# Performance work log

Measured on AMD Instinct MI355X. Metric: run time of the kernel, lower is better.

## Reference

```python
import jax, jax.numpy as jnp
import numpy as np

HIDDEN = 768
E_ROUTED = 32
K_ACT = 4
E_SHARED = 8
RANK = 64
FFN_ROUTED = HIDDEN * 2
FFN_SHARED = HIDDEN * 3


def setup_inputs() -> dict:
    key = jax.random.key(0)
    ks = jax.random.split(key, 8)
    s = 0.02
    return {
        "x": jax.random.normal(ks[0], (2, 2048, HIDDEN), dtype=jnp.float32),
        # shared experts: SwiGLU (gate, up, down), stacked over experts
        "shared_wg": jax.random.normal(ks[1], (E_SHARED, HIDDEN, FFN_SHARED), dtype=jnp.float32) * s,
        "shared_wu": jax.random.normal(ks[2], (E_SHARED, HIDDEN, FFN_SHARED), dtype=jnp.float32) * s,
        "shared_wd": jax.random.normal(ks[3], (E_SHARED, FFN_SHARED, HIDDEN), dtype=jnp.float32) * s,
        # routed experts: Linear -> GELU -> Linear, stacked
        "routed_w1": jax.random.normal(ks[4], (E_ROUTED, HIDDEN, FFN_ROUTED), dtype=jnp.float32) * s,
        "routed_w2": jax.random.normal(ks[5], (E_ROUTED, FFN_ROUTED, HIDDEN), dtype=jnp.float32) * s,
        # low-rank router
        "router_down": jax.random.normal(ks[6], (HIDDEN, RANK), dtype=jnp.float32) * s,
        "router_up": jax.random.normal(ks[7], (RANK, E_ROUTED), dtype=jnp.float32) * s,
    }


def reference(x, shared_wg, shared_wu, shared_wd, routed_w1, routed_w2, router_down, router_up):
    B, S, D = x.shape
    xf = x.reshape(-1, D)  # [T, D]

    # shared experts (SwiGLU), averaged
    g = jnp.einsum('td,edh->eth', xf, shared_wg)
    u = jnp.einsum('td,edh->eth', xf, shared_wu)
    sh = jnp.einsum('eth,ehd->etd', jax.nn.silu(g) * u, shared_wd)
    shared_output = sh.mean(axis=0)  # [T, D] (sum / num_shared_expert)

    # low-rank router + top-k
    router_logits = (xf @ router_down) @ router_up  # [T, E]
    routing_weights, selected = jax.lax.top_k(router_logits, K_ACT)  # [T, K]
    routing_weights = jax.nn.softmax(routing_weights, axis=-1)

    # dense all-expert FFN (faithful to source), then gather top-k (== one-hot einsum)
    h = jnp.einsum('td,edh->eth', xf, routed_w1)
    expert_outputs = jnp.einsum('eth,ehd->etd', jax.nn.gelu(h, approximate=False), routed_w2)  # [E,T,D]
    sel_out = jnp.take_along_axis(expert_outputs.transpose(1, 0, 2), selected[:, :, None], axis=1)  # [T,K,D]
    routed_output = jnp.einsum('tkd,tk->td', sel_out, routing_weights)

    output = (shared_output + routed_output).reshape(B, S, D)

    # aux losses
    counts = jnp.bincount(selected.reshape(-1), length=E_ROUTED).astype(jnp.float32)
    load_balance_loss = jnp.var(counts, ddof=1)  # torch .var() is unbiased
    probs = jax.nn.softmax(router_logits, axis=-1)
    router_entropy = -(probs * jnp.log(probs + 1e-10)).sum(-1).mean()
    shared_norm = jnp.linalg.norm(shared_output, axis=-1).mean()
    routed_norm = jnp.linalg.norm(routed_output, axis=-1).mean()
    balance_loss = jnp.abs(shared_norm - routed_norm)

    return output, load_balance_loss, router_entropy, balance_loss
```

## Files before the change

kernel.cpp:

```cpp
#include <hip/hip_runtime.h>
#include <hip/hip_bf16.h>
#include <math.h>


#define T_TOK 4096
#define DHID 768
#define NE_R 32
#define NE_S 8
#define F_S 2304
#define F_R 1536
#define MAXROWS 20480
#define MAX_TILES 160

typedef float f32x4 __attribute__((ext_vector_type(4)));
typedef short s16x8 __attribute__((ext_vector_type(8)));

__device__ __forceinline__ short f2bf(float f) {
  union { float f; unsigned u; } v; v.f = f;
  unsigned r = v.u + 0x7fffu + ((v.u >> 16) & 1u);
  return (short)(r >> 16);
}

#define GLD16(gsrc, ldst)                                                     \
  __builtin_amdgcn_global_load_lds(                                           \
      (const __attribute__((address_space(1))) void*)(gsrc),                  \
      (__attribute__((address_space(3))) void*)(ldst), 16, 0, 0)

__global__ __launch_bounds__(256) void cvt_x_kernel(const float* __restrict__ in,
    short* __restrict__ out, int* __restrict__ tlist, float* __restrict__ wslot,
    int* __restrict__ counts, int* __restrict__ cursor) {
  int i = blockIdx.x * 256 + threadIdx.x;
  if (i < T_TOK * DHID / 4) {
    float4 v = ((const float4*)in)[i];
    short4 o;
    o.x = f2bf(v.x); o.y = f2bf(v.y); o.z = f2bf(v.z); o.w = f2bf(v.w);
    ((short4*)out)[i] = o;
  }
  if (i < MAXROWS) { tlist[i] = 0; wslot[i] = 0.f; }
  if (i < 32) { counts[i] = 0; cursor[i] = 0; }
}

__device__ __forceinline__ void tile_transpose(const float* in, short* out,
                                               int R, int C, long ldo,
                                               int r0, int c0) {
  __shared__ float tile[64][65];
  int tx = threadIdx.x & 63, ty = threadIdx.x >> 6;
#pragma unroll
  for (int i = 0; i < 64; i += 4)
    tile[ty + i][tx] = in[(size_t)(r0 + ty + i) * C + (c0 + tx)];
  __syncthreads();
  int u = threadIdx.x & 15, v = threadIdx.x >> 4;
#pragma unroll
  for (int i = 0; i < 64; i += 16) {
    int c = v + i;
    short4 o;
    o.x = f2bf(tile[4 * u + 0][c]); o.y = f2bf(tile[4 * u + 1][c]);
    o.z = f2bf(tile[4 * u + 2][c]); o.w = f2bf(tile[4 * u + 3][c]);
    *(short4*)&out[(size_t)(c0 + c) * ldo + (r0 + 4 * u)] = o;
  }
}

__global__ __launch_bounds__(256) void transpose_shared(
    const float* __restrict__ swg, const float* __restrict__ swu,
    const float* __restrict__ swd, short* __restrict__ wgT,
    short* __restrict__ wuT, short* __restrict__ wdT) {
  int bid = blockIdx.x;
  const float* in; short* out; int R, C, nbx; long ldo;
  if (bid < 3456)      { in = swg; out = wgT; R = DHID; C = F_S; ldo = DHID; nbx = 36; }
  else if (bid < 6912) { bid -= 3456; in = swu; out = wuT; R = DHID; C = F_S; ldo = DHID; nbx = 36; }
  else                 { bid -= 6912; in = swd; out = wdT; R = F_S; C = DHID; ldo = F_S; nbx = 12; }
  int per = nbx * (R / 64);
  int b = bid / per, rem = bid % per;
  int c0 = (rem % nbx) * 64, r0 = (rem / nbx) * 64;
  tile_transpose(in + (size_t)b * R * C, out + (size_t)b * R * C, R, C, ldo, r0, c0);
}

__global__ __launch_bounds__(256) void transpose_routed(
    const float* __restrict__ rw1, const float* __restrict__ rw2,
    short* __restrict__ w1T, short* __restrict__ w2T) {
  int bid = blockIdx.x;
  const float* in; short* out; int R, C, nbx; long ldo;
  if (bid < 9216) { in = rw1; out = w1T; R = DHID; C = F_R; ldo = DHID; nbx = 24; }
  else            { bid -= 9216; in = rw2; out = w2T; R = F_R; C = DHID; ldo = F_R; nbx = 12; }
  int per = nbx * (R / 64);
  int b = bid / per, rem = bid % per;
  int c0 = (rem % nbx) * 64, r0 = (rem / nbx) * 64;
  tile_transpose(in + (size_t)b * R * C, out + (size_t)b * R * C, R, C, ldo, r0, c0);
}

__global__ __launch_bounds__(64) void router_kernel(const float* __restrict__ x,
    const float* __restrict__ rdown, const float* __restrict__ rup,
    int* __restrict__ sel, float* __restrict__ w4, int* __restrict__ counts,
    float* __restrict__ pent) {
  int t = blockIdx.x;
  int lane = threadIdx.x;
  __shared__ float xs[DHID];
  __shared__ float xrs[64];
  __shared__ float lg[32];
  const float* xt = x + (size_t)t * DHID;
  for (int i = lane; i < DHID; i += 64) xs[i] = xt[i];
  __syncthreads();
  float acc = 0.f;
#pragma unroll 8
  for (int d = 0; d < DHID; ++d) acc += xs[d] * rdown[d * 64 + lane];
  xrs[lane] = acc;
  __syncthreads();
  if (lane < 32) {
    float l = 0.f;
#pragma unroll 8
    for (int r = 0; r < 64; ++r) l += xrs[r] * rup[r * 32 + lane];
    lg[lane] = l;
  }
  __syncthreads();
  if (lane == 0) {
    int si[4]; float sv[4];
    unsigned taken = 0;
    for (int k = 0; k < 4; ++k) {
      float best = -3.4e38f; int bi = 0;
      for (int e = 0; e < 32; ++e)
        if (!((taken >> e) & 1u) && lg[e] > best) { best = lg[e]; bi = e; }
      taken |= 1u << bi; si[k] = bi; sv[k] = best;
    }
    float m = sv[0];
    float wv[4]; float zs = 0.f;
    for (int k = 0; k < 4; ++k) { wv[k] = __expf(sv[k] - m); zs += wv[k]; }
    for (int k = 0; k < 4; ++k) {
      sel[t * 4 + k] = si[k];
      w4[t * 4 + k] = wv[k] / zs;
      atomicAdd(&counts[si[k]], 1);
    }
    float Z = 0.f;
    for (int e = 0; e < 32; ++e) Z += __expf(lg[e] - m);
    float ent = 0.f;
    for (int e = 0; e < 32; ++e) {
      float p = __expf(lg[e] - m) / Z;
      ent -= p * logf(p + 1e-10f);
    }
    pent[t] = ent;
  }
}

__global__ __launch_bounds__(256) void build_kernel(const int* __restrict__ sel,
    const float* __restrict__ w4, const int* __restrict__ counts,
    int* __restrict__ cursor, int* __restrict__ tlist, float* __restrict__ wslot,
    int* __restrict__ pos, int* __restrict__ meta) {
  __shared__ int smeta[33];
  if (threadIdx.x == 0) {
    int acc = 0;
    for (int e = 0; e < 32; ++e) { smeta[e] = acc; acc += (counts[e] + 127) >> 7; }
    smeta[32] = acc;
    if (blockIdx.x == 0)
      for (int e = 0; e < 33; ++e) meta[e] = smeta[e];
  }
  __syncthreads();
  int t = blockIdx.x * 256 + threadIdx.x;
  if (t >= T_TOK) return;
#pragma unroll
  for (int k = 0; k < 4; ++k) {
    int e = sel[t * 4 + k];
    int slot = atomicAdd(&cursor[e], 1);
    int g = smeta[e] * 128 + slot;
    tlist[g] = t; wslot[g] = w4[t * 4 + k]; pos[t * 4 + k] = g;
  }
}

template<int MODE>
__global__ __launch_bounds__(256, 4) void gemm_k(
    const short* __restrict__ A, const short* __restrict__ B, const short* __restrict__ B2,
    short* __restrict__ outH, float* __restrict__ outF, const float* __restrict__ wslot,
    const int* __restrict__ meta, const int* __restrict__ tlist,
    int K, int lda, long zbstride, long ldo, long ocolz, long orowz, long acolz) {
  constexpr int BM = 128;
  constexpr int WM = 64, FM = 4, FN = 4;
  __shared__ short As[BM * 64];
  __shared__ short Bs[128 * 64];

  int tid = threadIdx.x;
  int wv = tid >> 6, lane = tid & 63;
  int wr = wv >> 1, wc = wv & 1;
  int lrow = lane & 15, kg = lane >> 4;
  int lrow7 = lrow & 7;
  int z = blockIdx.z;

  int bx = blockIdx.x, by = blockIdx.y;
  {
    int gx = gridDim.x, gy = gridDim.y;
    int nwg = gx * gy;
    int orig = by * gx + bx;
    int swz = (orig & 7) * (nwg >> 3) + (orig >> 3);
    if constexpr (MODE == 0 || MODE == 2) {
      bx = swz / gy; by = swz % gy;
    } else {
      bx = swz % gx; by = swz / gx;
    }
  }
  int n0 = bx * ((MODE == 0) ? 64 : 128);

  int eidx = z;
  int g0 = 0, m0 = by * BM;
  if constexpr (MODE == 1 || MODE == 3) {
    int total = meta[32];
    int ty = by;
    if (ty >= total) return;
    int e = 0;
    while (meta[e + 1] <= ty) ++e;
    eidx = e;
    g0 = ty * BM;
  }

  int srow = tid >> 3;
  int scol = ((tid & 7) ^ (srow & 7)) * 8;

  f32x4 acc[FM][FN] = {};

  constexpr int EPB = (MODE == 0 || MODE == 2) ? 2 : 1;
#pragma unroll 1
  for (int ei = 0; ei < EPB; ++ei) {
    int e = (EPB == 2) ? (z * 2 + ei) : eidx;
    const short* Bb = B + (size_t)e * zbstride + (size_t)n0 * K;

    const short *as0, *as1, *as2, *as3;
    {
      auto arow = [&](int row) -> const short* {
        if constexpr (MODE == 1) {
          return A + (size_t)tlist[g0 + row] * lda + scol;
        } else if constexpr (MODE == 2) {
          return A + ((size_t)(m0 + row)) * lda + (size_t)e * acolz + scol;
        } else if constexpr (MODE == 3) {
          return A + ((size_t)(g0 + row)) * lda + scol;
        } else {
          return A + ((size_t)(m0 + row)) * lda + scol;
        }
      };
      as0 = arow(srow); as1 = arow(32 + srow); as2 = arow(64 + srow); as3 = arow(96 + srow);
    }
    const short* bs0 = Bb + (size_t)srow * K + scol;
    const short* bs1 = bs0 + (size_t)32 * K;
    const short* bs2;
    const short* bs3;
    if constexpr (MODE == 0) {
      const short* B2b = B2 + (size_t)e * zbstride + (size_t)n0 * K;
      bs2 = B2b + (size_t)srow * K + scol;
      bs3 = bs2 + (size_t)32 * K;
    } else {
      bs2 = bs0 + (size_t)64 * K;
      bs3 = bs0 + (size_t)96 * K;
    }

    for (int kt = 0; kt < K; kt += 64) {
      GLD16(as0 + kt, As + (0 * 32 + wv * 8) * 64);
      GLD16(as1 + kt, As + (1 * 32 + wv * 8) * 64);
      GLD16(as2 + kt, As + (2 * 32 + wv * 8) * 64);
      GLD16(as3 + kt, As + (3 * 32 + wv * 8) * 64);
      GLD16(bs0 + kt, Bs + (0 * 32 + wv * 8) * 64);
      GLD16(bs1 + kt, Bs + (1 * 32 + wv * 8) * 64);
      GLD16(bs2 + kt, Bs + (2 * 32 + wv * 8) * 64);
      GLD16(bs3 + kt, Bs + (3 * 32 + wv * 8) * 64);
      __syncthreads();
#pragma unroll
      for (int ks = 0; ks < 2; ++ks) {
        int pc = ((ks * 4 + kg) ^ lrow7) * 8;
        s16x8 af[FM], bb[FN];
#pragma unroll
        for (int i = 0; i < FM; ++i)
          af[i] = *(const s16x8*)&As[(wr * WM + i * 16 + lrow) * 64 + pc];
#pragma unroll
        for (int j = 0; j < FN; ++j) {
          int brow;
          if constexpr (MODE == 0)
            brow = (j >= 2 ? 64 : 0) + wc * 32 + (j & 1) * 16 + lrow;
          else
            brow = wc * 64 + j * 16 + lrow;
          bb[j] = *(const s16x8*)&Bs[brow * 64 + pc];
        }
#pragma unroll
        for (int i = 0; i < FM; ++i)
#pragma unroll
          for (int j = 0; j < FN; ++j)
            acc[i][j] = __builtin_amdgcn_mfma_f32_16x16x32_bf16(af[i], bb[j], acc[i][j], 0, 0, 0);
      }
      __syncthreads();
    }

    if constexpr (MODE == 0) {
#pragma unroll
      for (int i = 0; i < FM; ++i) {
#pragma unroll
        for (int r = 0; r < 4; ++r) {
          int rl = wr * WM + i * 16 + kg * 4 + r;
#pragma unroll
          for (int jp = 0; jp < 2; ++jp) {
            int col = n0 + wc * 32 + jp * 16 + lrow;
            float g = acc[i][jp][r];
            float u = acc[i][jp + 2][r];
            float h = g / (1.f + __expf(-g)) * u;
            outH[(size_t)(m0 + rl) * ldo + (size_t)e * ocolz + col] = f2bf(h);
          }
        }
      }
#pragma unroll
      for (int i = 0; i < FM; ++i)
#pragma unroll
        for (int j = 0; j < FN; ++j)
          acc[i][j] = (f32x4){0.f, 0.f, 0.f, 0.f};
    }
  }

  if constexpr (MODE != 0) {
#pragma unroll
    for (int i = 0; i < FM; ++i) {
#pragma unroll
      for (int r = 0; r < 4; ++r) {
        int rl = wr * WM + i * 16 + kg * 4 + r;
        float wsc = 0.f;
        if constexpr (MODE == 1) wsc = wslot[g0 + rl];
#pragma unroll
        for (int j = 0; j < FN; ++j) {
          int col = n0 + wc * 64 + j * 16 + lrow;
          float v = acc[i][j][r];
          if constexpr (MODE == 1) {
            float vc = v * (0.7978845608f + 0.0356774081f * v * v);
            float h = v / (1.f + __expf(-2.f * vc)) * wsc;
            outH[(size_t)(g0 + rl) * ldo + col] = f2bf(h);
          } else if constexpr (MODE == 2) {
            outF[(size_t)z * orowz + (size_t)(m0 + rl) * DHID + col] = v;
          } else if constexpr (MODE == 3) {
            outF[(size_t)(g0 + rl) * DHID + col] = v;
          }
        }
      }
    }
  }
}

__global__ __launch_bounds__(256) void combine_kernel(const float* __restrict__ spart,
    const float* __restrict__ Y, const int* __restrict__ pos,
    float* __restrict__ out, float* __restrict__ pnorm) {
  int t = blockIdx.x, tid = threadIdx.x;
  int p0 = pos[t * 4], p1 = pos[t * 4 + 1], p2 = pos[t * 4 + 2], p3 = pos[t * 4 + 3];
  size_t base = (size_t)t * DHID;
  float s2 = 0.f, r2 = 0.f;
  for (int d = tid; d < DHID; d += 256) {
    float s = 0.f;
#pragma unroll
    for (int e = 0; e < 4; ++e) s += spart[(size_t)e * T_TOK * DHID + base + d];
    s *= 0.125f;
    float r = Y[(size_t)p0 * DHID + d] + Y[(size_t)p1 * DHID + d] +
              Y[(size_t)p2 * DHID + d] + Y[(size_t)p3 * DHID + d];
    out[base + d] = s + r;
    s2 += s * s; r2 += r * r;
  }
  for (int o = 32; o > 0; o >>= 1) { s2 += __shfl_down(s2, o); r2 += __shfl_down(r2, o); }
  __shared__ float red[8];
  int wv = tid >> 6, lane = tid & 63;
  if (lane == 0) { red[wv] = s2; red[4 + wv] = r2; }
  __syncthreads();
  if (tid == 0) {
    float st = red[0] + red[1] + red[2] + red[3];
    float rt = red[4] + red[5] + red[6] + red[7];
    pnorm[t] = sqrtf(st);
    pnorm[T_TOK + t] = sqrtf(rt);
  }
}

__global__ __launch_bounds__(256) void finalize_kernel(const int* __restrict__ counts,
    const float* __restrict__ pent, const float* __restrict__ pnorm, float* __restrict__ o) {
  int tid = threadIdx.x;
  float es = 0.f, ss = 0.f, rs = 0.f;
  for (int i = tid; i < T_TOK; i += 256) {
    es += pent[i]; ss += pnorm[i]; rs += pnorm[T_TOK + i];
  }
  float vs = 0.f;
  if (tid < 32) { float d = (float)counts[tid] - 512.f; vs = d * d; }
  for (int off = 32; off > 0; off >>= 1) {
    es += __shfl_down(es, off); ss += __shfl_down(ss, off);
    rs += __shfl_down(rs, off); vs += __shfl_down(vs, off);
  }
  __shared__ float red[16];
  int wv = tid >> 6, lane = tid & 63;
  if (lane == 0) { red[wv] = es; red[4 + wv] = ss; red[8 + wv] = rs; red[12 + wv] = vs; }
  __syncthreads();
  if (tid == 0) {
    es = red[0] + red[1] + red[2] + red[3];
    ss = red[4] + red[5] + red[6] + red[7];
    rs = red[8] + red[9] + red[10] + red[11];
    vs = red[12] + red[13] + red[14] + red[15];
    o[0] = vs / 31.f;
    o[1] = es / (float)T_TOK;
    o[2] = fabsf(ss - rs) / (float)T_TOK;
  }
}

extern "C" void kernel_launch(void* const* d_in, const int* in_sizes, int n_in,
                              void* d_out, int out_size, void* d_ws, size_t ws_size,
                              hipStream_t stream) {
  const float* x   = (const float*)d_in[0];
  const float* swg = (const float*)d_in[1];
  const float* swu = (const float*)d_in[2];
  const float* swd = (const float*)d_in[3];
  const float* rw1 = (const float*)d_in[4];
  const float* rw2 = (const float*)d_in[5];
  const float* rdn = (const float*)d_in[6];
  const float* rup = (const float*)d_in[7];
  float* fout = (float*)d_out;

  char* w = (char*)d_ws;
  size_t off = 0;
  auto take = [&](size_t bytes) { char* p = w + off; off = (off + bytes + 255) & ~(size_t)255; return p; };
  short* xbf   = (short*)take((size_t)T_TOK * DHID * 2);
  int*   sel   = (int*)  take((size_t)T_TOK * 4 * 4);
  float* w4    = (float*)take((size_t)T_TOK * 4 * 4);
  int*   pos   = (int*)  take((size_t)T_TOK * 4 * 4);
  int*   counts= (int*)  take(32 * 4);
  int*   cursor= (int*)  take(32 * 4);
  int*   meta  = (int*)  take(64 * 4);
  int*   tlist = (int*)  take((size_t)MAXROWS * 4);
  float* wslot = (float*)take((size_t)MAXROWS * 4);
  float* pent  = (float*)take((size_t)T_TOK * 4);
  float* pnorm = (float*)take((size_t)2 * T_TOK * 4);
  float* spart = (float*)take((size_t)4 * T_TOK * DHID * 4);
  char*  arena = w + off;

  short* wgT = (short*)arena;
  short* wuT = wgT + (size_t)NE_S * F_S * DHID;
  short* wdT = wuT + (size_t)NE_S * F_S * DHID;
  short* Hsh = wdT + (size_t)NE_S * F_S * DHID;
  float* Y   = (float*)arena;
  short* w1T = (short*)(arena + (size_t)MAXROWS * DHID * 4);
  short* w2T = w1T + (size_t)NE_R * F_R * DHID;
  short* Hr  = w2T + (size_t)NE_R * F_R * DHID;

  cvt_x_kernel<<<(T_TOK * DHID / 4 + 255) / 256, 256, 0, stream>>>(x, xbf, tlist, wslot, counts, cursor);
  router_kernel<<<T_TOK, 64, 0, stream>>>(x, rdn, rup, sel, w4, counts, pent);
  build_kernel<<<T_TOK / 256, 256, 0, stream>>>(sel, w4, counts, cursor, tlist, wslot, pos, meta);

  transpose_shared<<<10368, 256, 0, stream>>>(swg, swu, swd, wgT, wuT, wdT);
  gemm_k<0><<<dim3(F_S / 64, T_TOK / 128, NE_S / 2), 256, 0, stream>>>(
      xbf, wgT, wuT, Hsh, nullptr, nullptr, nullptr, nullptr,
      DHID, DHID, (long)F_S * DHID, (long)NE_S * F_S, (long)F_S, 0, 0);
  gemm_k<2><<<dim3(DHID / 128, T_TOK / 128, NE_S / 2), 256, 0, stream>>>(
      Hsh, wdT, nullptr, nullptr, spart, nullptr, nullptr, nullptr,
      F_S, NE_S * F_S, (long)DHID * F_S, DHID, 0, (long)T_TOK * DHID, (long)F_S);

  transpose_routed<<<18432, 256, 0, stream>>>(rw1, rw2, w1T, w2T);
  gemm_k<1><<<dim3(F_R / 128, MAX_TILES, 1), 256, 0, stream>>>(
      xbf, w1T, nullptr, Hr, nullptr, wslot, meta, tlist,
      DHID, DHID, (long)F_R * DHID, (long)F_R, 0, 0, 0);
  gemm_k<3><<<dim3(DHID / 128, MAX_TILES, 1), 256, 0, stream>>>(
      Hr, w2T, nullptr, nullptr, Y, nullptr, meta, tlist,
      F_R, F_R, (long)DHID * F_R, DHID, 0, 0, 0);

  combine_kernel<<<T_TOK, 256, 0, stream>>>(spart, Y, pos, fout, pnorm);
  finalize_kernel<<<1, 256, 0, stream>>>(counts, pent, pnorm, fout + (size_t)T_TOK * DHID);
}
```

Before: 934.7 us.

## Replace shared gate/up GEMM with 8-wave 256x256 double-buffered pipelined kernel

Adds a dedicated kernel for the shared-expert gate/up projection that uses 512 threads, a 256-row by 128-column tile (gate and up each), 128 KB of dynamic LDS with double buffering, and interleaves async global->LDS loads with MFMA quarters using explicit barriers, waitcnt and s_setprio. It replaces the generic MODE 0 path, which is removed from the templated GEMM, and launches one expert per z-slice. The goal is to overlap memory traffic with matrix-core work and raise arithmetic intensity through larger tiles. In exchange it runs at one workgroup per CU and depends on hand-tuned vmcnt counts, which are fragile if the issue order changes.

```diff
diff --git a/kernel.cpp b/kernel.cpp
--- a/kernel.cpp
+++ b/kernel.cpp
@@ -164,6 +164,179 @@
   }
 }
 
+#define RDA(p, qmlit)                                                         \
+  _Pragma("unroll")                                                           \
+  for (int mi = 0; mi < 4; ++mi)                                              \
+    _Pragma("unroll")                                                         \
+    for (int ks = 0; ks < 2; ++ks)                                            \
+      af[mi][ks] = *(const s16x8*)&As[(p) * 16384 +                           \
+          (wr * 128 + (qmlit) * 64 + mi * 16 + lrow) * 64 +                   \
+          ((ks * 4 + kg) ^ lrow7) * 8];
+
+#define RDB(p)                                                                \
+  _Pragma("unroll")                                                           \
+  for (int nj = 0; nj < 4; ++nj)                                              \
+    _Pragma("unroll")                                                         \
+    for (int ks = 0; ks < 2; ++ks)                                            \
+      bfz[nj][ks] = *(const s16x8*)&Bs[(p) * 16384 +                          \
+          ((nj >> 1) * 128 + wc * 32 + (nj & 1) * 16 + lrow) * 64 +           \
+          ((ks * 4 + kg) ^ lrow7) * 8];
+
+#define MFMAQ(qmlit, upofs)                                                   \
+  {                                                                           \
+    __builtin_amdgcn_s_setprio(1);                                            \
+    _Pragma("unroll")                                                         \
+    for (int mi = 0; mi < 4; ++mi)                                            \
+      _Pragma("unroll")                                                       \
+      for (int ks = 0; ks < 2; ++ks)                                          \
+        _Pragma("unroll")                                                     \
+        for (int nj = 0; nj < 2; ++nj)                                        \
+          acc[(qmlit) * 4 + mi][nj + (upofs)] =                               \
+              __builtin_amdgcn_mfma_f32_16x16x32_bf16(                        \
+                  af[mi][ks], bfz[nj + (upofs)][ks],                          \
+                  acc[(qmlit) * 4 + mi][nj + (upofs)], 0, 0, 0);              \
+    __builtin_amdgcn_s_setprio(0);                                            \
+  }
+
+#define ISSUE_A(s, h)                                                         \
+  { int sw = (s) >= NK ? (s) - NK : (s); int kt = sw * 64; int p = sw & 1;    \
+    GLD16(srcA[h][0] + kt, As + p * 16384 + (h) * 8192 + wv * 512);           \
+    GLD16(srcA[h][1] + kt, As + p * 16384 + (h) * 8192 + 4096 + wv * 512); }
+
+#define ISSUE_B(s, h)                                                         \
+  { int sw = (s) >= NK ? (s) - NK : (s); int kt = sw * 64; int p = sw & 1;    \
+    GLD16(srcB[h][0] + kt, Bs + p * 16384 + (h) * 8192 + wv * 512);           \
+    GLD16(srcB[h][1] + kt, Bs + p * 16384 + (h) * 8192 + 4096 + wv * 512); }
+
+#define BAR __builtin_amdgcn_s_barrier()
+#define LGKM0 asm volatile("s_waitcnt lgkmcnt(0)" ::: "memory")
+#define VM6 asm volatile("s_waitcnt vmcnt(6)" ::: "memory")
+#define VM0 asm volatile("s_waitcnt vmcnt(0)" ::: "memory")
+
+__global__ __launch_bounds__(512, 1) void gemm8_shared1(
+    const short* __restrict__ A, const short* __restrict__ Bg,
+    const short* __restrict__ Bu, short* __restrict__ outH) {
+  extern __shared__ short lds8[];
+  short* As = lds8;
+  short* Bs = lds8 + 32768;
+  constexpr int NK = DHID / 64;
+  constexpr int NITER = NK / 2;
+
+  int tid = threadIdx.x;
+  int wv = tid >> 6, lane = tid & 63;
+  int wr = wv >> 2, wc = wv & 3;
+  int lrow = lane & 15, kg = lane >> 4;
+  int lrow7 = lrow & 7;
+  int e = blockIdx.z;
+
+  int bx = blockIdx.x, by = blockIdx.y;
+  {
+    int gx = gridDim.x, gy = gridDim.y;
+    int nwg = gx * gy;
+    int orig = by * gx + bx;
+    int swz = (orig & 7) * (nwg >> 3) + (orig >> 3);
+    bx = swz / gy; by = swz % gy;
+  }
+  int n0 = bx * 128;
+  int m0 = by * 256;
+
+  const short* srcA[2][2];
+  const short* srcB[2][2];
+  {
+    const short* gb = Bg + (size_t)e * F_S * DHID + (size_t)n0 * DHID;
+    const short* ub = Bu + (size_t)e * F_S * DHID + (size_t)n0 * DHID;
+#pragma unroll
+    for (int l = 0; l < 2; ++l) {
+      int c = l * 512 + tid;
+      int row = c >> 3;
+      int sc = ((c & 7) ^ (row & 7)) * 8;
+      srcA[0][l] = A + (size_t)(m0 + row) * DHID + sc;
+      srcA[1][l] = A + (size_t)(m0 + 128 + row) * DHID + sc;
+      srcB[0][l] = gb + (size_t)row * DHID + sc;
+      srcB[1][l] = ub + (size_t)row * DHID + sc;
+    }
+  }
+
+  s16x8 af[4][2], bfz[4][2];
+  f32x4 acc[8][4] = {};
+
+  ISSUE_B(0, 0); ISSUE_B(0, 1); ISSUE_A(0, 0); ISSUE_A(0, 1);
+  ISSUE_B(1, 0); ISSUE_B(1, 1); ISSUE_A(1, 0);
+  VM6; BAR;
+
+#pragma unroll 1
+  for (int it = 0; it < NITER; ++it) {
+    int t = 2 * it, u = t + 1;
+    RDA(0, 0) RDB(0)
+    ISSUE_A(u, 1);
+    BAR; LGKM0;
+    MFMAQ(0, 0)
+    BAR;
+    ISSUE_B(t + 2, 0);
+    BAR;
+    MFMAQ(0, 2)
+    BAR;
+    RDA(0, 1)
+    ISSUE_B(t + 2, 1);
+    BAR; LGKM0;
+    MFMAQ(1, 0)
+    BAR;
+    ISSUE_A(t + 2, 0);
+    BAR;
+    MFMAQ(1, 2)
+    VM6;
+    BAR;
+    RDA(1, 0) RDB(1)
+    ISSUE_A(t + 2, 1);
+    BAR; LGKM0;
+    MFMAQ(0, 0)
+    BAR;
+    ISSUE_B(t + 3, 0);
+    BAR;
+    MFMAQ(0, 2)
+    BAR;
+    RDA(1, 1)
+    ISSUE_B(t + 3, 1);
+    BAR; LGKM0;
+    MFMAQ(1, 0)
+    BAR;
+    ISSUE_A(t + 3, 0);
+    BAR;
+    MFMAQ(1, 2)
+    VM6;
+    BAR;
+  }
+  VM0;
+
+  const long ldo = (long)NE_S * F_S;
+#pragma unroll
+  for (int qm = 0; qm < 2; ++qm)
+#pragma unroll
+    for (int mi = 0; mi < 4; ++mi)
+#pragma unroll
+      for (int r = 0; r < 4; ++r) {
+        int row = m0 + wr * 128 + qm * 64 + mi * 16 + kg * 4 + r;
+#pragma unroll
+        for (int nj = 0; nj < 2; ++nj) {
+          float g = acc[qm * 4 + mi][nj][r];
+          float uu = acc[qm * 4 + mi][nj + 2][r];
+          float h = g / (1.f + __expf(-g)) * uu;
+          int col = n0 + wc * 32 + nj * 16 + lrow;
+          outH[(size_t)row * ldo + (size_t)e * F_S + col] = f2bf(h);
+        }
+      }
+}
+
+#undef RDA
+#undef RDB
+#undef MFMAQ
+#undef ISSUE_A
+#undef ISSUE_B
+#undef BAR
+#undef LGKM0
+#undef VM6
+#undef VM0
+
 template<int MODE>
 __global__ __launch_bounds__(256, 4) void gemm_k(
     const short* __restrict__ A, const short* __restrict__ B, const short* __restrict__ B2,
@@ -188,13 +361,13 @@
     int nwg = gx * gy;
     int orig = by * gx + bx;
     int swz = (orig & 7) * (nwg >> 3) + (orig >> 3);
-    if constexpr (MODE == 0 || MODE == 2) {
+    if constexpr (MODE == 2) {
       bx = swz / gy; by = swz % gy;
     } else {
       bx = swz % gx; by = swz / gx;
     }
   }
-  int n0 = bx * ((MODE == 0) ? 64 : 128);
+  int n0 = bx * 128;
 
   int eidx = z;
   int g0 = 0, m0 = by * BM;
@@ -213,10 +386,10 @@
 
   f32x4 acc[FM][FN] = {};
 
-  constexpr int EPB = (MODE == 0 || MODE == 2) ? 2 : 1;
+  constexpr int EPB = (MODE == 2) ? 2 : 1;
 #pragma unroll 1
   for (int ei = 0; ei < EPB; ++ei) {
-    int e = (EPB == 2) ? (z * 2 + ei) : eidx;
+    int e = (MODE == 2) ? (z * 2 + ei) : eidx;
     const short* Bb = B + (size_t)e * zbstride + (size_t)n0 * K;
 
     const short *as0, *as1, *as2, *as3;
@@ -226,26 +399,16 @@
           return A + (size_t)tlist[g0 + row] * lda + scol;
         } else if constexpr (MODE == 2) {
           return A + ((size_t)(m0 + row)) * lda + (size_t)e * acolz + scol;
-        } else if constexpr (MODE == 3) {
+        } else {
           return A + ((size_t)(g0 + row)) * lda + scol;
-        } else {
-          return A + ((size_t)(m0 + row)) * lda + scol;
         }
       };
       as0 = arow(srow); as1 = arow(32 + srow); as2 = arow(64 + srow); as3 = arow(96 + srow);
     }
     const short* bs0 = Bb + (size_t)srow * K + scol;
     const short* bs1 = bs0 + (size_t)32 * K;
-    const short* bs2;
-    const short* bs3;
-    if constexpr (MODE == 0) {
-      const short* B2b = B2 + (size_t)e * zbstride + (size_t)n0 * K;
-      bs2 = B2b + (size_t)srow * K + scol;
-      bs3 = bs2 + (size_t)32 * K;
-    } else {
-      bs2 = bs0 + (size_t)64 * K;
-      bs3 = bs0 + (size_t)96 * K;
-    }
+    const short* bs2 = bs0 + (size_t)64 * K;
+    const short* bs3 = bs0 + (size_t)96 * K;
 
     for (int kt = 0; kt < K; kt += 64) {
       GLD16(as0 + kt, As + (0 * 32 + wv * 8) * 64);
@@ -265,14 +428,8 @@
         for (int i = 0; i < FM; ++i)
           af[i] = *(const s16x8*)&As[(wr * WM + i * 16 + lrow) * 64 + pc];
 #pragma unroll
-        for (int j = 0; j < FN; ++j) {
-          int brow;
-          if constexpr (MODE == 0)
-            brow = (j >= 2 ? 64 : 0) + wc * 32 + (j & 1) * 16 + lrow;
-          else
-            brow = wc * 64 + j * 16 + lrow;
-          bb[j] = *(const s16x8*)&Bs[brow * 64 + pc];
-        }
+        for (int j = 0; j < FN; ++j)
+          bb[j] = *(const s16x8*)&Bs[(wc * 64 + j * 16 + lrow) * 64 + pc];
 #pragma unroll
         for (int i = 0; i < FM; ++i)
 #pragma unroll
@@ -281,52 +438,27 @@
       }
       __syncthreads();
     }
-
-    if constexpr (MODE == 0) {
-#pragma unroll
-      for (int i = 0; i < FM; ++i) {
-#pragma unroll
-        for (int r = 0; r < 4; ++r) {
-          int rl = wr * WM + i * 16 + kg * 4 + r;
-#pragma unroll
-          for (int jp = 0; jp < 2; ++jp) {
-            int col = n0 + wc * 32 + jp * 16 + lrow;
-            float g = acc[i][jp][r];
-            float u = acc[i][jp + 2][r];
-            float h = g / (1.f + __expf(-g)) * u;
-            outH[(size_t)(m0 + rl) * ldo + (size_t)e * ocolz + col] = f2bf(h);
-          }
-        }
-      }
-#pragma unroll
-      for (int i = 0; i < FM; ++i)
-#pragma unroll
-        for (int j = 0; j < FN; ++j)
-          acc[i][j] = (f32x4){0.f, 0.f, 0.f, 0.f};
-    }
-  }
-
-  if constexpr (MODE != 0) {
-#pragma unroll
-    for (int i = 0; i < FM; ++i) {
-#pragma unroll
-      for (int r = 0; r < 4; ++r) {
-        int rl = wr * WM + i * 16 + kg * 4 + r;
-        float wsc = 0.f;
-        if constexpr (MODE == 1) wsc = wslot[g0 + rl];
-#pragma unroll
-        for (int j = 0; j < FN; ++j) {
-          int col = n0 + wc * 64 + j * 16 + lrow;
-          float v = acc[i][j][r];
-          if constexpr (MODE == 1) {
-            float vc = v * (0.7978845608f + 0.0356774081f * v * v);
-            float h = v / (1.f + __expf(-2.f * vc)) * wsc;
-            outH[(size_t)(g0 + rl) * ldo + col] = f2bf(h);
-          } else if constexpr (MODE == 2) {
-            outF[(size_t)z * orowz + (size_t)(m0 + rl) * DHID + col] = v;
-          } else if constexpr (MODE == 3) {
-            outF[(size_t)(g0 + rl) * DHID + col] = v;
-          }
+  }
+
+#pragma unroll
+  for (int i = 0; i < FM; ++i) {
+#pragma unroll
+    for (int r = 0; r < 4; ++r) {
+      int rl = wr * WM + i * 16 + kg * 4 + r;
+      float wsc = 0.f;
+      if constexpr (MODE == 1) wsc = wslot[g0 + rl];
+#pragma unroll
+      for (int j = 0; j < FN; ++j) {
+        int col = n0 + wc * 64 + j * 16 + lrow;
+        float v = acc[i][j][r];
+        if constexpr (MODE == 1) {
+          float vc = v * (0.7978845608f + 0.0356774081f * v * v);
+          float h = v / (1.f + __expf(-2.f * vc)) * wsc;
+          outH[(size_t)(g0 + rl) * ldo + col] = f2bf(h);
+        } else if constexpr (MODE == 2) {
+          outF[(size_t)z * orowz + (size_t)(m0 + rl) * DHID + col] = v;
+        } else if constexpr (MODE == 3) {
+          outF[(size_t)(g0 + rl) * DHID + col] = v;
         }
       }
     }
@@ -403,6 +535,9 @@
   const float* rdn = (const float*)d_in[6];
   const float* rup = (const float*)d_in[7];
   float* fout = (float*)d_out;
+
+  (void)hipFuncSetAttribute((const void*)gemm8_shared1,
+                            hipFuncAttributeMaxDynamicSharedMemorySize, 131072);
 
   char* w = (char*)d_ws;
   size_t off = 0;
@@ -435,9 +570,8 @@
   build_kernel<<<T_TOK / 256, 256, 0, stream>>>(sel, w4, counts, cursor, tlist, wslot, pos, meta);
 
   transpose_shared<<<10368, 256, 0, stream>>>(swg, swu, swd, wgT, wuT, wdT);
-  gemm_k<0><<<dim3(F_S / 64, T_TOK / 128, NE_S / 2), 256, 0, stream>>>(
-      xbf, wgT, wuT, Hsh, nullptr, nullptr, nullptr, nullptr,
-      DHID, DHID, (long)F_S * DHID, (long)NE_S * F_S, (long)F_S, 0, 0);
+  gemm8_shared1<<<dim3(F_S / 128, T_TOK / 256, NE_S), 512, 131072, stream>>>(
+      xbf, wgT, wuT, Hsh);
   gemm_k<2><<<dim3(DHID / 128, T_TOK / 128, NE_S / 2), 256, 0, stream>>>(
       Hsh, wdT, nullptr, nullptr, spart, nullptr, nullptr, nullptr,
       F_S, NE_S * F_S, (long)DHID * F_S, DHID, 0, (long)T_TOK * DHID, (long)F_S);
```

New measurement: 860.4 us. 1.09x faster.
